# Kernel tuning notes

Measured on AMD Instinct MI355X. Metric: run time of the kernel, lower is better.

Reference implementation:

```python
import jax, jax.numpy as jnp
import numpy as np

B, N, DIM = 8, 1024, 768
HEADS, HEAD_DIM = 12, 64
INNER = HEADS * HEAD_DIM  # 768
SCALE = HEAD_DIM ** -0.5


def setup_inputs() -> dict:
    key = jax.random.key(0)
    k1, k2, k3, k4 = jax.random.split(key, 4)
    x = jax.random.normal(k1, (B, N, DIM), dtype=jnp.float32)
    # nn.Linear weights, stored as (in, out) for x @ W
    w_qkv = jax.random.normal(k2, (DIM, 3 * INNER), dtype=jnp.float32) * (DIM ** -0.5)
    w_out = jax.random.normal(k3, (INNER, DIM), dtype=jnp.float32) * (INNER ** -0.5)
    b_out = jax.random.normal(k4, (DIM,), dtype=jnp.float32) * 0.02
    return {"x": x, "w_qkv": w_qkv, "w_out": w_out, "b_out": b_out}


def reference(x, w_qkv, w_out, b_out):
    qkv = jnp.einsum('bnd,de->bne', x, w_qkv)  # [B, N, 3*INNER]
    q, k, v = jnp.split(qkv, 3, axis=-1)
    # 'b n (h d) -> b h n d'
    def split_heads(t):
        return t.reshape(B, N, HEADS, HEAD_DIM).transpose(0, 2, 1, 3)
    q, k, v = split_heads(q), split_heads(k), split_heads(v)
    score = jnp.einsum('bhnd,bhmd->bhnm', q, k) * SCALE  # [B, H, N, N]
    # Faithful to torch nn.Softmax() with dim=None on a 4D tensor: legacy
    # behavior applies softmax over dim=1 (the HEADS axis), NOT the key axis.
    attention = jax.nn.softmax(score, axis=1)
    out = jnp.einsum('bhnm,bhmd->bhnd', attention, v)  # [B, H, N, D]
    out = out.transpose(0, 2, 1, 3).reshape(B, N, INNER)  # 'b h n d -> b n (h d)'
    return jnp.einsum('bne,ed->bnd', out, w_out) + b_out
```

## Files before the change

### kernel.cpp

```cpp
#include <hip/hip_runtime.h>

typedef float  f32x4  __attribute__((ext_vector_type(4)));
typedef short  bf16x8 __attribute__((ext_vector_type(8)));

#define MFMA16(a, b, c) __builtin_amdgcn_mfma_f32_16x16x32_bf16((a), (b), (c), 0, 0, 0)

#define GLL16(g, l) __builtin_amdgcn_global_load_lds(                      \
    (const __attribute__((address_space(1))) void*)(g),                    \
    (__attribute__((address_space(3))) void*)(l), 16, 0, 0)

__device__ __forceinline__ short f2bf(float f) {
    union { float f; unsigned u; } a; a.f = f;
    unsigned r = a.u + 0x7fffu + ((a.u >> 16) & 1u);
    return (short)(r >> 16);
}
__device__ __forceinline__ float bf2f(unsigned short u) {
    union { unsigned u; float f; } a; a.u = ((unsigned)u) << 16; return a.f;
}

#define Bb   8
#define Nn   1024
#define DIM  768
#define HH   12
#define HD   64
#define INNER 768
#define SCALE 0.125f
#define SCL2E 0.18033688011112042f

__global__ void cast_to_bf16(const float* __restrict__ in, short* __restrict__ out, int n4) {
    int i = blockIdx.x * 256 + threadIdx.x;
    if (i >= n4) return;
    float4 f = reinterpret_cast<const float4*>(in)[i];
    unsigned lo = (unsigned)(unsigned short)f2bf(f.x) | ((unsigned)(unsigned short)f2bf(f.y) << 16);
    unsigned hi = (unsigned)(unsigned short)f2bf(f.z) | ((unsigned)(unsigned short)f2bf(f.w) << 16);
    reinterpret_cast<uint2*>(out)[i] = make_uint2(lo, hi);
}

__global__ void transpose_cast(const float* __restrict__ w, short* __restrict__ wt,
                               int rows, int cols) {
    int idx = blockIdx.x * 256 + threadIdx.x;
    if (idx >= rows * cols) return;
    int c = idx / rows;
    int k = idx - c * rows;
    wt[idx] = f2bf(w[k * cols + c]);
}

#define STAGE(ksv, bv)                                                      \
  { const int kc_ = (ksv) << 5;                                             \
    GLL16(A  + aoff + kc_,                  &As[bv][lch]);                  \
    GLL16(A  + aoff + (size_t)64 * K + kc_, &As[bv][2048 + lch]);           \
    GLL16(Bt + boff + kc_,                  &Bs[bv][lch]);                  \
    GLL16(Bt + boff + (size_t)64 * K + kc_, &Bs[bv][2048 + lch]); }

#define PHASE(VM, DO_STAGE)                                                 \
  {                                                                         \
    bf16x8 af[4], bfr[4];                                                   \
    _Pragma("unroll") for (int t = 0; t < 4; t++)                           \
      af[t] = *reinterpret_cast<const bf16x8*>(                             \
          &As[bi][(wrow * 64 + t * 16 + l16) * 32 + swo]);                  \
    _Pragma("unroll") for (int t = 0; t < 4; t++)                           \
      bfr[t] = *reinterpret_cast<const bf16x8*>(                            \
          &Bs[bi][(wcol * 64 + t * 16 + l16) * 32 + swo]);                  \
    if (DO_STAGE) { STAGE(ks + 2, bn); }                                    \
    asm volatile("s_waitcnt vmcnt(" #VM ")" ::: "memory");                  \
    __builtin_amdgcn_s_barrier();                                           \
    asm volatile("s_waitcnt lgkmcnt(0)" ::: "memory");                      \
    __builtin_amdgcn_sched_barrier(0);                                      \
    __builtin_amdgcn_s_setprio(1);                                          \
    _Pragma("unroll") for (int rt = 0; rt < 4; rt++)                        \
      _Pragma("unroll") for (int ct = 0; ct < 4; ct++)                      \
        acc[rt][ct] = MFMA16(af[rt], bfr[ct], acc[rt][ct]);                 \
    __builtin_amdgcn_s_setprio(0);                                          \
    __builtin_amdgcn_s_barrier();                                           \
  }

template <int MODE>
__global__ __launch_bounds__(256, 3)
void gemm128(const short* __restrict__ A, const short* __restrict__ Bt, int K,
             short* __restrict__ qb, short* __restrict__ kb, short* __restrict__ vtb,
             float* __restrict__ outp, const float* __restrict__ bias) {
    __shared__ __align__(16) short As[3][128 * 32];
    __shared__ __align__(16) short Bs[3][128 * 32];

    const int tid  = threadIdx.x;
    const int lane = tid & 63, wv = tid >> 6;
    const int wrow = wv >> 1, wcol = wv & 1;
    const int quad = lane >> 4, l16 = lane & 15;

    const int bid = blockIdx.x;
    const int m0 = (((bid & 7) << 3) | ((bid >> 3) & 7)) << 7;
    const int n0 = (bid >> 6) << 7;

    const int row64 = (wv << 4) + (lane >> 2);
    const int gu = (lane & 3) ^ ((lane >> 3) & 3);
    const size_t aoff = (size_t)(m0 + row64) * K + gu * 8;
    const size_t boff = (size_t)(n0 + row64) * K + gu * 8;
    const int lch = wv * 512;

    f32x4 acc[4][4];
#pragma unroll
    for (int i = 0; i < 4; i++)
#pragma unroll
        for (int j = 0; j < 4; j++) acc[i][j] = (f32x4){0.f, 0.f, 0.f, 0.f};

    const int swo = (quad ^ ((l16 >> 1) & 3)) * 8;

    const int NK = K >> 5;

    STAGE(0, 0);
    STAGE(1, 1);
    asm volatile("s_waitcnt vmcnt(4)" ::: "memory");
    __builtin_amdgcn_s_barrier();

    int bi = 0, bn = 2;
    int ks = 0;
    for (; ks < NK - 2; ks++) {
        PHASE(4, true);
        bi = (bi == 2) ? 0 : bi + 1;
        bn = (bn == 2) ? 0 : bn + 1;
    }
    PHASE(0, false);
    bi = (bi == 2) ? 0 : bi + 1;
    PHASE(0, false);

#pragma unroll
    for (int rt = 0; rt < 4; rt++) {
#pragma unroll
        for (int ct = 0; ct < 4; ct++) {
            const int c = n0 + wcol * 64 + ct * 16 + l16;
#pragma unroll
            for (int reg = 0; reg < 4; reg++) {
                const int r = m0 + wrow * 64 + rt * 16 + quad * 4 + reg;
                const float v = acc[rt][ct][reg];
                if (MODE == 0) {
                    const int b = r >> 10, n = r & 1023;
                    const int which = (c >= 1536) ? 2 : (c >= 768 ? 1 : 0);
                    const int cc = c - which * 768;
                    const int h = cc >> 6, d = cc & 63;
                    const int bh = b * HH + h;
                    const short bv = f2bf(v);
                    if (which == 0)      qb[(bh << 16) + (n << 6) + d] = bv;
                    else if (which == 1) kb[(bh << 16) + (n << 6) + d] = bv;
                    else                 vtb[(bh << 16) + (d << 10) + n] = bv;
                } else {
                    outp[(size_t)r * 768 + c] = v + bias[c];
                }
            }
        }
    }
}

__global__ __launch_bounds__(512, 4)
void attn_den5(const short* __restrict__ qb, const short* __restrict__ kb,
               short* __restrict__ invp) {
    __shared__ __align__(16) short Qs[2][128 * 64];
    __shared__ __align__(16) short Ks[2][128 * 64];

    const int tid = threadIdx.x, lane = tid & 63, wv = tid >> 6;
    const int wrow = wv >> 2, wcol = wv & 3;
    const int quad = lane >> 4, l16 = lane & 15;
    const int bid = blockIdx.x;
    const int b = bid & 7;
    const int nmt = bid >> 3;
    const int n0 = (nmt >> 3) << 7;
    const int m0 = (nmt & 7) << 7;

    const int r8 = lane >> 3;
    const int gu = (lane & 7) ^ r8;
    const int qo0 = (n0 + wv * 8 + r8) * 64 + gu * 8;
    const int qo1 = qo0 + 64 * 64;
    const int ko0 = (m0 + wv * 8 + r8) * 64 + gu * 8;
    const int ko1 = ko0 + 64 * 64;
    const int lc0 = wv * 512;
    const int lc1 = 4096 + wv * 512;

    f32x4 den[4][2];
#pragma unroll
    for (int i = 0; i < 4; i++)
#pragma unroll
        for (int j = 0; j < 2; j++) den[i][j] = (f32x4){0.f, 0.f, 0.f, 0.f};
    const f32x4 z = (f32x4){0.f, 0.f, 0.f, 0.f};

    {
        const short* qh = qb + ((size_t)(b * HH) << 16);
        const short* kh = kb + ((size_t)(b * HH) << 16);
        GLL16(qh + qo0, &Qs[0][lc0]);
        GLL16(qh + qo1, &Qs[0][lc1]);
        GLL16(kh + ko0, &Ks[0][lc0]);
        GLL16(kh + ko1, &Ks[0][lc1]);
    }

    for (int h = 0; h < HH; h++) {
        asm volatile("s_waitcnt vmcnt(0)" ::: "memory");
        __syncthreads();
        if (h < HH - 1) {
            const int pn = (h + 1) & 1;
            const short* qh = qb + ((size_t)(b * HH + h + 1) << 16);
            const short* kh = kb + ((size_t)(b * HH + h + 1) << 16);
            GLL16(qh + qo0, &Qs[pn][lc0]);
            GLL16(qh + qo1, &Qs[pn][lc1]);
            GLL16(kh + ko0, &Ks[pn][lc0]);
            GLL16(kh + ko1, &Ks[pn][lc1]);
        }
        const int pb = h & 1;
        const int sw0 = (quad ^ (l16 & 7)) * 8;

        bf16x8 aq[4][2], bk[2][2];
#pragma unroll
        for (int t = 0; t < 4; t++) {
            const int row = wrow * 64 + t * 16 + l16;
            aq[t][0] = *reinterpret_cast<bf16x8*>(&Qs[pb][row * 64 + sw0]);
            aq[t][1] = *reinterpret_cast<bf16x8*>(&Qs[pb][row * 64 + (sw0 ^ 32)]);
        }
#pragma unroll
        for (int t = 0; t < 2; t++) {
            const int row = wcol * 32 + t * 16 + l16;
            bk[t][0] = *reinterpret_cast<bf16x8*>(&Ks[pb][row * 64 + sw0]);
            bk[t][1] = *reinterpret_cast<bf16x8*>(&Ks[pb][row * 64 + (sw0 ^ 32)]);
        }
#pragma unroll
        for (int nt = 0; nt < 4; nt++)
#pragma unroll
            for (int mt = 0; mt < 2; mt++) {
                f32x4 s = MFMA16(aq[nt][0], bk[mt][0], z);
                s = MFMA16(aq[nt][1], bk[mt][1], s);
#pragma unroll
                for (int r = 0; r < 4; r++)
                    den[nt][mt][r] += __builtin_amdgcn_exp2f(s[r] * SCL2E);
            }
    }

#pragma unroll
    for (int nt = 0; nt < 4; nt++)
#pragma unroll
        for (int mt = 0; mt < 2; mt++) {
            const int ntg = (n0 >> 4) + wrow * 4 + nt;
            const int mtg = (m0 >> 4) + wcol * 2 + mt;
            ushort4 o;
            o.x = (unsigned short)f2bf(1.0f / den[nt][mt][0]);
            o.y = (unsigned short)f2bf(1.0f / den[nt][mt][1]);
            o.z = (unsigned short)f2bf(1.0f / den[nt][mt][2]);
            o.w = (unsigned short)f2bf(1.0f / den[nt][mt][3]);
            *reinterpret_cast<ushort4*>(&invp[(((b * 64 + ntg) * 64 + mtg) * 64 + lane) * 4]) = o;
        }
}

__global__ __launch_bounds__(256, 4)
void attn_pv2(const short* __restrict__ qb, const short* __restrict__ kb,
              const short* __restrict__ vtb, const short* __restrict__ invp,
              short* __restrict__ attn_out) {
    __shared__ __align__(16) short Ks[2][32 * 72];
    __shared__ __align__(16) short Vs[2][64 * 40];
    __shared__ __align__(16) short Ps[4][32 * 40];

    const int tid = threadIdx.x, lane = tid & 63, wv = tid >> 6;
    const int quad = lane >> 4, l16 = lane & 15;
    const int bid = blockIdx.x;
    const int b = bid & 7;
    const int r = bid >> 3;
    const int n4 = r / 12;
    const int h = r - n4 * 12;
    const int nb = n4 << 7;
    const int bh = b * HH + h;

    bf16x8 aq[2][2];
#pragma unroll
    for (int nt = 0; nt < 2; nt++) {
        const short* qp = qb + (bh << 16) + ((nb + wv * 32 + nt * 16 + l16) << 6) + quad * 8;
        aq[nt][0] = *reinterpret_cast<const bf16x8*>(qp);
        aq[nt][1] = *reinterpret_cast<const bf16x8*>(qp + 32);
    }

    const f32x4 z = (f32x4){0.f, 0.f, 0.f, 0.f};
    f32x4 O[2][4];
#pragma unroll
    for (int nt = 0; nt < 2; nt++)
#pragma unroll
        for (int d = 0; d < 4; d++) O[nt][d] = z;

    const int krow = tid >> 3, koff = (tid & 7) * 8;
    const int vrow = tid >> 2, voff = (tid & 3) * 8;

    uint4 kreg = *reinterpret_cast<const uint4*>(kb + (bh << 16) + (krow << 6) + koff);
    uint4 vreg = *reinterpret_cast<const uint4*>(vtb + (bh << 16) + (vrow << 10) + voff);

    for (int it = 0; it < 32; it++) {
        const int p = it & 1;
        *reinterpret_cast<uint4*>(&Ks[p][krow * 72 + koff]) = kreg;
        *reinterpret_cast<uint4*>(&Vs[p][vrow * 40 + voff]) = vreg;
        __syncthreads();
        if (it < 31) {
            const int m1 = (it + 1) << 5;
            kreg = *reinterpret_cast<const uint4*>(kb + (bh << 16) + ((m1 + krow) << 6) + koff);
            vreg = *reinterpret_cast<const uint4*>(vtb + (bh << 16) + (vrow << 10) + m1 + voff);
        }
        const int m0 = it << 5;

#pragma unroll
        for (int mh = 0; mh < 2; mh++) {
            const bf16x8 k0 = *reinterpret_cast<bf16x8*>(&Ks[p][(mh * 16 + l16) * 72 + quad * 8]);
            const bf16x8 k1 = *reinterpret_cast<bf16x8*>(&Ks[p][(mh * 16 + l16) * 72 + quad * 8 + 32]);
            const int mt = (m0 >> 4) + mh;
#pragma unroll
            for (int nt = 0; nt < 2; nt++) {
                f32x4 s = MFMA16(aq[nt][0], k0, z);
                s = MFMA16(aq[nt][1], k1, s);
                const int ntg = (nb >> 4) + wv * 2 + nt;
                const ushort4 iv = *reinterpret_cast<const ushort4*>(
                    &invp[(((b * 64 + ntg) * 64 + mt) * 64 + lane) * 4]);
                Ps[wv][(nt * 16 + quad * 4 + 0) * 40 + mh * 16 + l16] = f2bf(__expf(s[0] * SCALE) * bf2f(iv.x));
                Ps[wv][(nt * 16 + quad * 4 + 1) * 40 + mh * 16 + l16] = f2bf(__expf(s[1] * SCALE) * bf2f(iv.y));
                Ps[wv][(nt * 16 + quad * 4 + 2) * 40 + mh * 16 + l16] = f2bf(__expf(s[2] * SCALE) * bf2f(iv.z));
                Ps[wv][(nt * 16 + quad * 4 + 3) * 40 + mh * 16 + l16] = f2bf(__expf(s[3] * SCALE) * bf2f(iv.w));
            }
        }
        __threadfence_block();

        bf16x8 pa[2];
#pragma unroll
        for (int nt = 0; nt < 2; nt++)
            pa[nt] = *reinterpret_cast<bf16x8*>(&Ps[wv][(nt * 16 + l16) * 40 + quad * 8]);
#pragma unroll
        for (int dch = 0; dch < 4; dch++) {
            const bf16x8 vf = *reinterpret_cast<bf16x8*>(&Vs[p][(dch * 16 + l16) * 40 + quad * 8]);
#pragma unroll
            for (int nt = 0; nt < 2; nt++)
                O[nt][dch] = MFMA16(pa[nt], vf, O[nt][dch]);
        }
    }

#pragma unroll
    for (int nt = 0; nt < 2; nt++)
#pragma unroll
        for (int dch = 0; dch < 4; dch++) {
            const int col = h * 64 + dch * 16 + l16;
#pragma unroll
            for (int reg = 0; reg < 4; reg++) {
                const int n = nb + wv * 32 + nt * 16 + quad * 4 + reg;
                attn_out[(size_t)((b << 10) + n) * 768 + col] = f2bf(O[nt][dch][reg]);
            }
        }
}

extern "C" void kernel_launch(void* const* d_in, const int* in_sizes, int n_in,
                              void* d_out, int out_size, void* d_ws, size_t ws_size,
                              hipStream_t stream) {
    const float* x     = (const float*)d_in[0];
    const float* w_qkv = (const float*)d_in[1];
    const float* w_out = (const float*)d_in[2];
    const float* b_out = (const float*)d_in[3];
    float* out = (float*)d_out;

    short* xb   = (short*)d_ws;
    short* wT1  = xb  + 8192 * 768;
    short* wT2  = wT1 + 2304 * 768;
    short* qb   = wT2 + 768 * 768;
    short* kb   = qb  + 96 * 65536;
    short* vtb  = kb  + 96 * 65536;
    short* attn = vtb + 96 * 65536;
    short* invp = attn + 8192 * 768;

    cast_to_bf16<<<6144, 256, 0, stream>>>(x, xb, (8192 * 768) / 4);
    transpose_cast<<<(2304 * 768) / 256, 256, 0, stream>>>(w_qkv, wT1, 768, 2304);
    transpose_cast<<<(768 * 768) / 256, 256, 0, stream>>>(w_out, wT2, 768, 768);

    gemm128<0><<<1152, 256, 0, stream>>>(
        xb, wT1, 768, qb, kb, vtb, nullptr, nullptr);

    attn_den5<<<512, 512, 0, stream>>>(qb, kb, invp);
    attn_pv2<<<768, 256, 0, stream>>>(qb, kb, vtb, invp, attn);

    gemm128<1><<<384, 256, 0, stream>>>(
        attn, wT2, 768, nullptr, nullptr, nullptr, out, b_out);
}
```

Baseline: 234.7 us.

## Load K and V fragments directly from global memory in attn_pv, dropping LDS staging

The PV attention kernel no longer stages K and V tiles through double-buffered shared memory with block-wide barriers. Each wave now reads its MFMA operand fragments straight from global memory, relying on L1/L2 caching since all four waves read the same K/V. The exponent is computed with the hardware exp2 builtin on a prescaled log2e constant, and the occupancy hint drops from 4 to 3 blocks. This removes the __syncthreads and LDS traffic, but adds redundant global loads per wave and loses the software prefetch, so load latency is now exposed.

```diff
diff --git a/kernel.cpp b/kernel.cpp
--- a/kernel.cpp
+++ b/kernel.cpp
@@ -245,12 +245,10 @@
         }
 }
 
-__global__ __launch_bounds__(256, 4)
-void attn_pv2(const short* __restrict__ qb, const short* __restrict__ kb,
+__global__ __launch_bounds__(256, 3)
+void attn_pv3(const short* __restrict__ qb, const short* __restrict__ kb,
               const short* __restrict__ vtb, const short* __restrict__ invp,
               short* __restrict__ attn_out) {
-    __shared__ __align__(16) short Ks[2][32 * 72];
-    __shared__ __align__(16) short Vs[2][64 * 40];
     __shared__ __align__(16) short Ps[4][32 * 40];
 
     const int tid = threadIdx.x, lane = tid & 63, wv = tid >> 6;
@@ -278,28 +276,17 @@
 #pragma unroll
         for (int d = 0; d < 4; d++) O[nt][d] = z;
 
-    const int krow = tid >> 3, koff = (tid & 7) * 8;
-    const int vrow = tid >> 2, voff = (tid & 3) * 8;
-
-    uint4 kreg = *reinterpret_cast<const uint4*>(kb + (bh << 16) + (krow << 6) + koff);
-    uint4 vreg = *reinterpret_cast<const uint4*>(vtb + (bh << 16) + (vrow << 10) + voff);
+    const short* kfr = kb  + (bh << 16) + (l16 << 6)  + quad * 8;
+    const short* vfr = vtb + (bh << 16) + (l16 << 10) + quad * 8;
 
     for (int it = 0; it < 32; it++) {
-        const int p = it & 1;
-        *reinterpret_cast<uint4*>(&Ks[p][krow * 72 + koff]) = kreg;
-        *reinterpret_cast<uint4*>(&Vs[p][vrow * 40 + voff]) = vreg;
-        __syncthreads();
-        if (it < 31) {
-            const int m1 = (it + 1) << 5;
-            kreg = *reinterpret_cast<const uint4*>(kb + (bh << 16) + ((m1 + krow) << 6) + koff);
-            vreg = *reinterpret_cast<const uint4*>(vtb + (bh << 16) + (vrow << 10) + m1 + voff);
-        }
         const int m0 = it << 5;
 
 #pragma unroll
         for (int mh = 0; mh < 2; mh++) {
-            const bf16x8 k0 = *reinterpret_cast<bf16x8*>(&Ks[p][(mh * 16 + l16) * 72 + quad * 8]);
-            const bf16x8 k1 = *reinterpret_cast<bf16x8*>(&Ks[p][(mh * 16 + l16) * 72 + quad * 8 + 32]);
+            const short* kp = kfr + ((m0 + mh * 16) << 6);
+            const bf16x8 k0 = *reinterpret_cast<const bf16x8*>(kp);
+            const bf16x8 k1 = *reinterpret_cast<const bf16x8*>(kp + 32);
             const int mt = (m0 >> 4) + mh;
 #pragma unroll
             for (int nt = 0; nt < 2; nt++) {
@@ -308,10 +295,10 @@
                 const int ntg = (nb >> 4) + wv * 2 + nt;
                 const ushort4 iv = *reinterpret_cast<const ushort4*>(
                     &invp[(((b * 64 + ntg) * 64 + mt) * 64 + lane) * 4]);
-                Ps[wv][(nt * 16 + quad * 4 + 0) * 40 + mh * 16 + l16] = f2bf(__expf(s[0] * SCALE) * bf2f(iv.x));
-                Ps[wv][(nt * 16 + quad * 4 + 1) * 40 + mh * 16 + l16] = f2bf(__expf(s[1] * SCALE) * bf2f(iv.y));
-                Ps[wv][(nt * 16 + quad * 4 + 2) * 40 + mh * 16 + l16] = f2bf(__expf(s[2] * SCALE) * bf2f(iv.z));
-                Ps[wv][(nt * 16 + quad * 4 + 3) * 40 + mh * 16 + l16] = f2bf(__expf(s[3] * SCALE) * bf2f(iv.w));
+                Ps[wv][(nt * 16 + quad * 4 + 0) * 40 + mh * 16 + l16] = f2bf(__builtin_amdgcn_exp2f(s[0] * SCL2E) * bf2f(iv.x));
+                Ps[wv][(nt * 16 + quad * 4 + 1) * 40 + mh * 16 + l16] = f2bf(__builtin_amdgcn_exp2f(s[1] * SCL2E) * bf2f(iv.y));
+                Ps[wv][(nt * 16 + quad * 4 + 2) * 40 + mh * 16 + l16] = f2bf(__builtin_amdgcn_exp2f(s[2] * SCL2E) * bf2f(iv.z));
+                Ps[wv][(nt * 16 + quad * 4 + 3) * 40 + mh * 16 + l16] = f2bf(__builtin_amdgcn_exp2f(s[3] * SCL2E) * bf2f(iv.w));
             }
         }
         __threadfence_block();
@@ -322,7 +309,7 @@
             pa[nt] = *reinterpret_cast<bf16x8*>(&Ps[wv][(nt * 16 + l16) * 40 + quad * 8]);
 #pragma unroll
         for (int dch = 0; dch < 4; dch++) {
-            const bf16x8 vf = *reinterpret_cast<bf16x8*>(&Vs[p][(dch * 16 + l16) * 40 + quad * 8]);
+            const bf16x8 vf = *reinterpret_cast<const bf16x8*>(vfr + (dch << 14) + m0);
 #pragma unroll
             for (int nt = 0; nt < 2; nt++)
                 O[nt][dch] = MFMA16(pa[nt], vf, O[nt][dch]);
@@ -368,7 +355,7 @@
         xb, wT1, 768, qb, kb, vtb, nullptr, nullptr);
 
     attn_den5<<<512, 512, 0, stream>>>(qb, kb, invp);
-    attn_pv2<<<768, 256, 0, stream>>>(qb, kb, vtb, invp, attn);
+    attn_pv3<<<768, 256, 0, stream>>>(qb, kb, vtb, invp, attn);
 
     gemm128<1><<<384, 256, 0, stream>>>(
         attn, wT2, 768, nullptr, nullptr, nullptr, out, b_out);
```

Result: slower. 288.9 us (+23.1%).
